# Kernel optimization log

Hardware: AMD Instinct MI355X
Metric: run time of the kernel (lower is better)

Reference implementation:

```python
import jax, jax.numpy as jnp
import numpy as np

D_MODEL = 1024


def setup_inputs() -> dict:
    key = jax.random.key(0)
    ks = jax.random.split(key, 11)
    B, S, D = 4, 2048, D_MODEL
    scale = 1.0 / np.sqrt(D)
    inp = {
        "query": jax.random.normal(ks[0], (B, S, D), dtype=jnp.float32),
        "key": jax.random.normal(ks[1], (B, S, D), dtype=jnp.float32),
        "value": jax.random.normal(ks[2], (B, S, D), dtype=jnp.float32),
        # nn.Linear weights stored torch-style as [out, in]; y = x @ W.T + b
        "Wq": jax.random.normal(ks[3], (D, D), dtype=jnp.float32) * scale,
        "bq": jnp.zeros((D,), dtype=jnp.float32),
        "Wk": jax.random.normal(ks[4], (D, D), dtype=jnp.float32) * scale,
        "bk": jnp.zeros((D,), dtype=jnp.float32),
        "Wv": jax.random.normal(ks[5], (D, D), dtype=jnp.float32) * scale,
        "bv": jnp.zeros((D,), dtype=jnp.float32),
        "Wo": jax.random.normal(ks[6], (D, D), dtype=jnp.float32) * scale,
        "bo": jnp.zeros((D,), dtype=jnp.float32),
    }
    return inp


def reference(query, key, value, Wq, bq, Wk, bk, Wv, bv, Wo, bo):
    d_model = query.shape[-1]
    q = jnp.einsum("bsd,ed->bse", query, Wq) + bq  # q_proj
    k = jnp.einsum("bsd,ed->bse", key, Wk) + bk    # k_proj
    v = jnp.einsum("bsd,ed->bse", value, Wv) + bv  # v_proj
    # scores scaled by sqrt(d_model) (single head: full d_model, per original code)
    scores = jnp.einsum("bqe,bke->bqk", q, k) / jnp.sqrt(jnp.asarray(d_model, q.dtype))
    attn = jax.nn.softmax(scores, axis=-1)
    # dropout is identity in eval mode
    out = jnp.einsum("bqk,bke->bqe", attn, v)
    out = jnp.einsum("bqe,fe->bqf", out, Wo) + bo  # out_proj
    return out
```

## Files before the change

kernel.cpp:

```cpp
#include <hip/hip_runtime.h>
#include <stdint.h>


typedef __bf16  bf16x8 __attribute__((ext_vector_type(8)));
typedef float   f32x4  __attribute__((ext_vector_type(4)));
typedef unsigned int u32x4 __attribute__((ext_vector_type(4)));

__device__ __forceinline__ unsigned short bf16_rne(float f) {
  unsigned int u = __builtin_bit_cast(unsigned int, f);
  u += 0x7FFFu + ((u >> 16) & 1u);
  return (unsigned short)(u >> 16);
}
__device__ __forceinline__ unsigned int pack2(float a, float b) {
  return (unsigned int)bf16_rne(a) | ((unsigned int)bf16_rne(b) << 16);
}
__device__ __forceinline__ void async16(const unsigned short* g, unsigned short* l) {
  __builtin_amdgcn_global_load_lds(
      (const __attribute__((address_space(1))) unsigned int*)g,
      (__attribute__((address_space(3))) unsigned int*)l,
      16, 0, 0);
}

#define FENCE() asm volatile("" ::: "memory")
#define BAR()   __builtin_amdgcn_s_barrier()
#define MFMA_   __builtin_amdgcn_mfma_f32_16x16x32_bf16

#define T1_ARGS() \
  const int xcd = orig & 7, loc = orig >> 3; \
  const int qq  = nwg >> 3, rr = nwg & 7; \
  const int w   = (xcd < rr ? xcd * (qq + 1) : rr * (qq + 1) + (xcd - rr) * qq) + loc; \
  const int bxi = w % nx; \
  const int byi = (w / nx) % ny; \
  const int bzi = w / (nx * ny);

template<int OUT_F32>
__device__ __forceinline__ void gbody256(
    unsigned short* __restrict__ lds,
    const unsigned short* __restrict__ A, const unsigned short* __restrict__ B,
    void* __restrict__ Cp,
    int K, int lda, int ldb, int ldc,
    long sAz, long sBz, long sCz, long sBiasZ,
    float scale, const float* __restrict__ bias, int bias_mode,
    int nx, int ny, int nwg, int orig)
{
  T1_ARGS();

  const int tid  = threadIdx.x;
  const int lane = tid & 63;
  const int wid  = tid >> 6;
  const int bm   = byi * 256;
  const int bn   = bxi * 256;
  const long z   = bzi;

  const unsigned short* Az = A + z * sAz;
  const unsigned short* Bz = B + z * sBz;

  const int wm  = wid >> 2;
  const int wn  = wid & 3;
  const int al  = lane & 15;
  const int ah  = lane >> 4;
  const int al7 = lane & 7;

  const int swz = ((lane & 7) ^ ((lane >> 3) & 7)) << 3;
  const unsigned short* Apt = Az + (long)(bm + wid * 32 + (lane >> 3)) * lda + swz;
  const unsigned short* Bpt = Bz + (long)(bn + wid * 32 + (lane >> 3)) * ldb + swz;
  const long a8 = (long)lda * 8, b8 = (long)ldb * 8;

#define SALL(kt, stg) { \
    const unsigned short* pa_ = Apt + ((long)(kt) << 6); \
    const unsigned short* pb_ = Bpt + ((long)(kt) << 6); \
    async16(pa_,          (stg) + wid * 2048);        \
    async16(pa_ + a8,     (stg) + wid * 2048 + 512);  \
    async16(pa_ + 2 * a8, (stg) + wid * 2048 + 1024); \
    async16(pa_ + 3 * a8, (stg) + wid * 2048 + 1536); \
    async16(pb_,          (stg) + 16384 + wid * 2048);        \
    async16(pb_ + b8,     (stg) + 16384 + wid * 2048 + 512);  \
    async16(pb_ + 2 * b8, (stg) + 16384 + wid * 2048 + 1024); \
    async16(pb_ + 3 * b8, (stg) + 16384 + wid * 2048 + 1536); }

#define LDA2(v0, v1, mm) { const int r_ = (wm * 128 + (mm) * 16 + al) * 64; \
    v0 = *(const bf16x8*)&as[r_ + ((ah ^ al7) << 3)]; \
    v1 = *(const bf16x8*)&as[r_ + (((4 | ah) ^ al7) << 3)]; }
#define LDB2(v0, v1, nn) { const int r_ = (wn * 64 + (nn) * 16 + al) * 64; \
    v0 = *(const bf16x8*)&bs[r_ + ((ah ^ al7) << 3)]; \
    v1 = *(const bf16x8*)&bs[r_ + (((4 | ah) ^ al7) << 3)]; }
#define MM2(mi, ni, av0, av1, bv0, bv1) { \
    acc[mi][ni] = MFMA_(av0, bv0, acc[mi][ni], 0, 0, 0); \
    acc[mi][ni] = MFMA_(av1, bv1, acc[mi][ni], 0, 0, 0); }

  f32x4 acc[8][4] = {};
  const int nkt = K >> 6;

  SALL(0, lds);

  int cur = 0;
  for (int t = 0; t < nkt; ++t) {
    asm volatile("s_waitcnt vmcnt(0)" ::: "memory");
    BAR(); FENCE();

    const unsigned short* as  = lds + cur * 32768;
    const unsigned short* bs  = as + 16384;
    unsigned short*       stg = lds + (cur ^ 1) * 32768;

    bf16x8 a0k0, a0k1, a1k0, a1k1, a2k0, a2k1, a3k0, a3k1;
    bf16x8 a4k0, a4k1, a5k0, a5k1, a6k0, a6k1, a7k0, a7k1;
    bf16x8 b0k0, b0k1, b1k0, b1k1, b2k0, b2k1, b3k0, b3k1;
    LDA2(a0k0, a0k1, 0); LDA2(a1k0, a1k1, 1); LDA2(a2k0, a2k1, 2); LDA2(a3k0, a3k1, 3);
    LDA2(a4k0, a4k1, 4); LDA2(a5k0, a5k1, 5); LDA2(a6k0, a6k1, 6); LDA2(a7k0, a7k1, 7);
    LDB2(b0k0, b0k1, 0); LDB2(b1k0, b1k1, 1); LDB2(b2k0, b2k1, 2); LDB2(b3k0, b3k1, 3);

    if (t + 1 < nkt) SALL(t + 1, stg);

    MM2(0,0, a0k0,a0k1, b0k0,b0k1); MM2(1,0, a1k0,a1k1, b0k0,b0k1);
    MM2(2,0, a2k0,a2k1, b0k0,b0k1); MM2(3,0, a3k0,a3k1, b0k0,b0k1);
    MM2(4,0, a4k0,a4k1, b0k0,b0k1); MM2(5,0, a5k0,a5k1, b0k0,b0k1);
    MM2(6,0, a6k0,a6k1, b0k0,b0k1); MM2(7,0, a7k0,a7k1, b0k0,b0k1);
    MM2(0,1, a0k0,a0k1, b1k0,b1k1); MM2(1,1, a1k0,a1k1, b1k0,b1k1);
    MM2(2,1, a2k0,a2k1, b1k0,b1k1); MM2(3,1, a3k0,a3k1, b1k0,b1k1);
    MM2(4,1, a4k0,a4k1, b1k0,b1k1); MM2(5,1, a5k0,a5k1, b1k0,b1k1);
    MM2(6,1, a6k0,a6k1, b1k0,b1k1); MM2(7,1, a7k0,a7k1, b1k0,b1k1);
    MM2(0,2, a0k0,a0k1, b2k0,b2k1); MM2(1,2, a1k0,a1k1, b2k0,b2k1);
    MM2(2,2, a2k0,a2k1, b2k0,b2k1); MM2(3,2, a3k0,a3k1, b2k0,b2k1);
    MM2(4,2, a4k0,a4k1, b2k0,b2k1); MM2(5,2, a5k0,a5k1, b2k0,b2k1);
    MM2(6,2, a6k0,a6k1, b2k0,b2k1); MM2(7,2, a7k0,a7k1, b2k0,b2k1);
    MM2(0,3, a0k0,a0k1, b3k0,b3k1); MM2(1,3, a1k0,a1k1, b3k0,b3k1);
    MM2(2,3, a2k0,a2k1, b3k0,b3k1); MM2(3,3, a3k0,a3k1, b3k0,b3k1);
    MM2(4,3, a4k0,a4k1, b3k0,b3k1); MM2(5,3, a5k0,a5k1, b3k0,b3k1);
    MM2(6,3, a6k0,a6k1, b3k0,b3k1); MM2(7,3, a7k0,a7k1, b3k0,b3k1);

    cur ^= 1;
  }

  #pragma unroll
  for (int m = 0; m < 8; ++m) {
    #pragma unroll
    for (int n = 0; n < 4; ++n) {
      #pragma unroll
      for (int j = 0; j < 4; ++j) {
        const int grow = bm + wm * 128 + m * 16 + ah * 4 + j;
        const int gcol = bn + wn * 64 + n * 16 + al;
        float v = acc[m][n][j] * scale;
        if (bias_mode == 1)      v += bias[z * sBiasZ + gcol];
        else if (bias_mode == 2) v += bias[z * sBiasZ + grow];
        const long idx = z * sCz + (long)grow * ldc + gcol;
        if (OUT_F32) ((float*)Cp)[idx] = v;
        else         ((unsigned short*)Cp)[idx] = bf16_rne(v);
      }
    }
  }
}

template<int OUT_F32>
__device__ __forceinline__ void gbody8(
    unsigned short* __restrict__ lds,
    const unsigned short* __restrict__ A, const unsigned short* __restrict__ B,
    void* __restrict__ Cp,
    int K, int lda, int ldb, int ldc,
    long sAz, long sBz, long sCz, long sBiasZ,
    float scale, const float* __restrict__ bias, int bias_mode,
    int nx, int ny, int nwg, int orig)
{
  T1_ARGS();

  const int tid  = threadIdx.x;
  const int lane = tid & 63;
  const int wid  = tid >> 6;
  const int bm   = byi * 256;
  const int bn   = bxi * 128;
  const long z   = bzi;

  const unsigned short* Az = A + z * sAz;
  const unsigned short* Bz = B + z * sBz;

  const int wr  = (wid >> 1) * 64;
  const int wc  = (wid & 1)  * 64;
  const int al  = lane & 15;
  const int ah  = lane >> 4;
  const int al7 = lane & 7;

  const int swz = ((lane & 7) ^ ((lane >> 3) & 7)) << 3;
  const unsigned short* Apt = Az + (long)(bm + wid * 32 + (lane >> 3)) * lda + swz;
  const unsigned short* Bpt = Bz + (long)(bn + wid * 16 + (lane >> 3)) * ldb + swz;
  const long a8 = (long)lda * 8, b8 = (long)ldb * 8;

  f32x4 acc[4][4] = {};
  const int nkt = K >> 6;

#define STAGE_AB(kt, stg) { \
    const unsigned short* a_ = Apt + ((long)(kt) << 6); \
    const unsigned short* b_ = Bpt + ((long)(kt) << 6); \
    async16(a_,          (stg) + wid * 2048);        \
    async16(a_ + a8,     (stg) + wid * 2048 + 512);  \
    async16(a_ + 2 * a8, (stg) + wid * 2048 + 1024); \
    async16(a_ + 3 * a8, (stg) + wid * 2048 + 1536); \
    async16(b_,          (stg) + 16384 + wid * 1024); \
    async16(b_ + b8,     (stg) + 16384 + wid * 1024 + 512); }

#define LDA_(m) { const int r_ = (wr + (m) * 16 + al) * 64; \
    af##m##0 = *(const bf16x8*)&as[r_ + ((ah ^ al7) << 3)]; \
    af##m##1 = *(const bf16x8*)&as[r_ + (((4 | ah) ^ al7) << 3)]; }
#define LDB_(n) { const int r_ = (wc + (n) * 16 + al) * 64; \
    bf##n##0 = *(const bf16x8*)&bs[r_ + ((ah ^ al7) << 3)]; \
    bf##n##1 = *(const bf16x8*)&bs[r_ + (((4 | ah) ^ al7) << 3)]; }
#define MM(m, n) { \
    acc[m][n] = MFMA_(af##m##0, bf##n##0, acc[m][n], 0, 0, 0); \
    acc[m][n] = MFMA_(af##m##1, bf##n##1, acc[m][n], 0, 0, 0); }

  STAGE_AB(0, lds);
  STAGE_AB(1, lds + 24576);

  int cur = 0;
  for (int t = 0; t < nkt; ++t) {
    const int stb  = (cur >= 1) ? cur - 1 : cur + 2;

    if (t + 1 < nkt) asm volatile("s_waitcnt vmcnt(6)" ::: "memory");
    else             asm volatile("s_waitcnt vmcnt(0)" ::: "memory");
    BAR(); FENCE();

    const unsigned short* as  = lds + cur * 24576;
    const unsigned short* bs  = as + 16384;
    unsigned short*       stg = lds + stb * 24576;

    bf16x8 af00, af01, af10, af11, af20, af21, af30, af31;
    bf16x8 bf00, bf01, bf10, bf11, bf20, bf21, bf30, bf31;
    LDA_(0); LDA_(1); LDA_(2); LDA_(3);
    LDB_(0); LDB_(1); LDB_(2); LDB_(3);

    if (t + 2 < nkt) STAGE_AB(t + 2, stg);

    MM(0,0); MM(1,0); MM(2,0); MM(3,0);
    MM(0,1); MM(1,1); MM(2,1); MM(3,1);
    MM(0,2); MM(1,2); MM(2,2); MM(3,2);
    MM(0,3); MM(1,3); MM(2,3); MM(3,3);

    cur = (cur == 2) ? 0 : cur + 1;
  }

  #pragma unroll
  for (int m = 0; m < 4; ++m) {
    #pragma unroll
    for (int n = 0; n < 4; ++n) {
      #pragma unroll
      for (int j = 0; j < 4; ++j) {
        const int grow = bm + wr + m * 16 + ah * 4 + j;
        const int gcol = bn + wc + n * 16 + al;
        float v = acc[m][n][j] * scale;
        if (bias_mode == 1)      v += bias[z * sBiasZ + gcol];
        else if (bias_mode == 2) v += bias[z * sBiasZ + grow];
        const long idx = z * sCz + (long)grow * ldc + gcol;
        if (OUT_F32) ((float*)Cp)[idx] = v;
        else         ((unsigned short*)Cp)[idx] = bf16_rne(v);
      }
    }
  }
}

template<int OUT_F32>
__global__ __launch_bounds__(512) void gemm256(
    const unsigned short* __restrict__ A, const unsigned short* __restrict__ B,
    void* __restrict__ Cp, int K, int lda, int ldb, int ldc,
    long sAz, long sBz, long sCz, long sBiasZ,
    float scale, const float* __restrict__ bias, int bias_mode)
{
  __shared__ unsigned short lds[2 * 32768];
  const int nx = gridDim.x, ny = gridDim.y;
  const int nwg = nx * ny * gridDim.z;
  const int orig = ((int)blockIdx.z * ny + blockIdx.y) * nx + blockIdx.x;
  gbody256<OUT_F32>(lds, A, B, Cp, K, lda, ldb, ldc, sAz, sBz, sCz, sBiasZ,
                    scale, bias, bias_mode, nx, ny, nwg, orig);
}

template<int OUT_F32>
__global__ __launch_bounds__(512) void gemm8(
    const unsigned short* __restrict__ A, const unsigned short* __restrict__ B,
    void* __restrict__ Cp, int K, int lda, int ldb, int ldc,
    long sAz, long sBz, long sCz, long sBiasZ,
    float scale, const float* __restrict__ bias, int bias_mode)
{
  __shared__ unsigned short lds[3 * 24576];
  const int nx = gridDim.x, ny = gridDim.y;
  const int nwg = nx * ny * gridDim.z;
  const int orig = ((int)blockIdx.z * ny + blockIdx.y) * nx + blockIdx.x;
  gbody8<OUT_F32>(lds, A, B, Cp, K, lda, ldb, ldc, sAz, sBz, sCz, sBiasZ,
                  scale, bias, bias_mode, nx, ny, nwg, orig);
}

__global__ __launch_bounds__(512) void dual_qk_vt(
    const unsigned short* __restrict__ qf, const unsigned short* __restrict__ Wb,
    unsigned short* __restrict__ q, const float* __restrict__ bqk,
    const unsigned short* __restrict__ Wv, const unsigned short* __restrict__ vf,
    unsigned short* __restrict__ vT, const float* __restrict__ bv)
{
  __shared__ unsigned short lds[3 * 24576];
  const int bid = blockIdx.x;
  if (bid < 256) {
    gbody256<0>(lds, qf, Wb, q, 1024, 1024, 1024, 1024,
                8388608L, 1048576L, 8388608L, 1024L, 1.0f, bqk, 1,
                4, 32, 256, bid);
  } else {
    gbody8<0>(lds, Wv, vf, vT, 1024, 1024, 1024, 8192,
              0L, 0L, 0L, 0L, 1.0f, bv, 2,
              64, 4, 256, bid - 256);
  }
}

__device__ __forceinline__ void cvt8(const float* in, unsigned short* out, long i) {
  f32x4 a = *(const f32x4*)(in + i * 8);
  f32x4 b = *(const f32x4*)(in + i * 8 + 4);
  u32x4 w;
  w[0] = pack2(a[0], a[1]); w[1] = pack2(a[2], a[3]);
  w[2] = pack2(b[0], b[1]); w[3] = pack2(b[2], b[3]);
  *(u32x4*)(out + i * 8) = w;
}

__global__ __launch_bounds__(256) void mega_cvt3(
    const float* __restrict__ wq, const float* __restrict__ wk,
    const float* __restrict__ wv, const float* __restrict__ wo,
    const float* __restrict__ query, const float* __restrict__ key_,
    const float* __restrict__ value,
    const float* __restrict__ bq, const float* __restrict__ bk,
    unsigned short* __restrict__ Wb, unsigned short* __restrict__ qf,
    unsigned short* __restrict__ kf, unsigned short* __restrict__ vf,
    float* __restrict__ bqk)
{
  const int b = blockIdx.x;
  if (b < 2048) {
    const long i = (long)(b & 511) * 256 + threadIdx.x;
    if (b < 512)        cvt8(wq, Wb,            i);
    else if (b < 1024)  cvt8(wk, Wb + 1048576,  i);
    else if (b < 1536)  cvt8(wv, Wb + 2097152,  i);
    else                cvt8(wo, Wb + 3145728,  i);
  } else if (b < 6144) {
    cvt8(query, qf, (long)(b - 2048) * 256 + threadIdx.x);
  } else if (b < 10240) {
    cvt8(key_,  kf, (long)(b - 6144) * 256 + threadIdx.x);
  } else if (b < 10248) {
    const int t = (b - 10240) * 256 + threadIdx.x;
    if (t < 1024) bqk[t] = bq[t];
    else          bqk[t] = bk[t - 1024];
  } else {
    cvt8(value, vf, (long)(b - 10248) * 256 + threadIdx.x);
  }
}

__global__ __launch_bounds__(256) void cvt_f32_bf16(
    const float* __restrict__ in, unsigned short* __restrict__ out, int n8)
{
  const int i = blockIdx.x * 256 + threadIdx.x;
  if (i >= n8) return;
  cvt8(in, out, i);
}

__global__ __launch_bounds__(256) void softmax_inplace(unsigned short* __restrict__ P) {
  const long row = blockIdx.x;
  unsigned short* pr = P + row * 2048;
  const int tid = threadIdx.x;

  u32x4 raw = *(const u32x4*)&pr[tid * 8];
  float s[8];
  #pragma unroll
  for (int i = 0; i < 4; ++i) {
    unsigned int u = raw[i];
    s[2 * i]     = __builtin_bit_cast(float, u << 16);
    s[2 * i + 1] = __builtin_bit_cast(float, u & 0xFFFF0000u);
  }
  float m = s[0];
  #pragma unroll
  for (int i = 1; i < 8; ++i) m = fmaxf(m, s[i]);
  #pragma unroll
  for (int off = 32; off >= 1; off >>= 1) m = fmaxf(m, __shfl_xor(m, off));

  __shared__ float redm[4], reds[4];
  const int wid = tid >> 6, lane = tid & 63;
  if (lane == 0) redm[wid] = m;
  __syncthreads();
  m = fmaxf(fmaxf(redm[0], redm[1]), fmaxf(redm[2], redm[3]));

  float e[8], sum = 0.f;
  #pragma unroll
  for (int i = 0; i < 8; ++i) { e[i] = __expf(s[i] - m); sum += e[i]; }
  #pragma unroll
  for (int off = 32; off >= 1; off >>= 1) sum += __shfl_xor(sum, off);
  if (lane == 0) reds[wid] = sum;
  __syncthreads();
  sum = reds[0] + reds[1] + reds[2] + reds[3];
  const float inv = 1.0f / sum;

  u32x4 outw;
  #pragma unroll
  for (int i = 0; i < 4; ++i) outw[i] = pack2(e[2 * i] * inv, e[2 * i + 1] * inv);
  *(u32x4*)&pr[tid * 8] = outw;
}

extern "C" void kernel_launch(void* const* d_in, const int* in_sizes, int n_in,
                              void* d_out, int out_size, void* d_ws, size_t ws_size,
                              hipStream_t stream) {
  const float* query = (const float*)d_in[0];
  const float* key_  = (const float*)d_in[1];
  const float* value = (const float*)d_in[2];
  const float* Wq    = (const float*)d_in[3];
  const float* bq    = (const float*)d_in[4];
  const float* Wk    = (const float*)d_in[5];
  const float* bk    = (const float*)d_in[6];
  const float* Wv    = (const float*)d_in[7];
  const float* bv    = (const float*)d_in[8];
  const float* Wo    = (const float*)d_in[9];
  const float* bo    = (const float*)d_in[10];

  unsigned short* ws = (unsigned short*)d_ws;
  unsigned short* qf = ws;
  unsigned short* kf = ws + 8388608;
  unsigned short* P  = ws;
  unsigned short* q  = ws + 16777216;
  unsigned short* vT = ws + 33554432;
  unsigned short* Wb = ws + 41943040;
  float*          bqk= (float*)(ws + 46137344);
  unsigned short* o  = q;

  const bool par = ws_size >= (size_t)(46141440 + 8388608) * 2;
  unsigned short* vf = par ? (ws + 46141440) : ws;

  const dim3 blk(256), blk8(512);

  mega_cvt3<<<dim3(par ? 14344 : 10248), blk, 0, stream>>>(
      Wq, Wk, Wv, Wo, query, key_, value, bq, bk, Wb, qf, kf, vf, bqk);

  if (par) {
    dual_qk_vt<<<dim3(512), blk8, 0, stream>>>(qf, Wb, q, bqk,
                                               Wb + 2097152, vf, vT, bv);
  } else {
    gemm256<0><<<dim3(4, 32, 2), blk8, 0, stream>>>(qf, Wb, q,
        1024, 1024, 1024, 1024, 8388608L, 1048576L, 8388608L, 1024L, 1.0f, bqk, 1);
    cvt_f32_bf16<<<dim3(4096), blk, 0, stream>>>(value, vf, 1048576);
    gemm8<0><<<dim3(64, 4, 1), blk8, 0, stream>>>(Wb + 2097152, vf, vT,
        1024, 1024, 1024, 8192, 0L, 0L, 0L, 0L, 1.0f, bv, 2);
  }

  gemm256<0><<<dim3(8, 8, 4), blk8, 0, stream>>>(q, q + 8388608, P,
      1024, 1024, 1024, 2048, 2097152L, 2097152L, 4194304L, 0L, 0.03125f, nullptr, 0);

  softmax_inplace<<<dim3(8192), blk, 0, stream>>>(P);

  gemm8<0><<<dim3(8, 8, 4), blk8, 0, stream>>>(P, vT, o,
      2048, 2048, 8192, 1024, 4194304L, 2048L, 2097152L, 0L, 1.0f, nullptr, 0);

  gemm8<1><<<dim3(8, 32, 1), blk8, 0, stream>>>(o, Wb + 3145728, d_out,
      1024, 1024, 1024, 1024, 0L, 0L, 0L, 0L, 1.0f, bo, 1);
}
```

Measured before the change: 200.9 us.

## Fold output projection into value by precomputing V·Woᵀ before attention

Uses associativity, (P·V)·Woᵀ = P·(V·Woᵀ), to fold the output projection into the value path. The V projection now yields row-major v. A new fused kernel computes the QK scores alongside the transposed product W2T = (V·Woᵀ)ᵀ, so the separate P·V and output-projection GEMMs become one P·W2T GEMM with bias, written in fp32 straight to the output. This removes one full GEMM launch and the round trip of the intermediate o tensor. The cost is an extra 8192x1024x1024 GEMM moved earlier and an added bf16 rounding of V·Woᵀ, which changes numerics slightly.

```diff
diff --git a/kernel.cpp b/kernel.cpp
--- a/kernel.cpp
+++ b/kernel.cpp
@@ -285,11 +285,11 @@
                   scale, bias, bias_mode, nx, ny, nwg, orig);
 }
 
-__global__ __launch_bounds__(512) void dual_qk_vt(
+__global__ __launch_bounds__(512) void dual_qk_v(
     const unsigned short* __restrict__ qf, const unsigned short* __restrict__ Wb,
     unsigned short* __restrict__ q, const float* __restrict__ bqk,
-    const unsigned short* __restrict__ Wv, const unsigned short* __restrict__ vf,
-    unsigned short* __restrict__ vT, const float* __restrict__ bv)
+    const unsigned short* __restrict__ vf, const unsigned short* __restrict__ Wv,
+    unsigned short* __restrict__ v, const float* __restrict__ bv)
 {
   __shared__ unsigned short lds[3 * 24576];
   const int bid = blockIdx.x;
@@ -298,8 +298,27 @@
                 8388608L, 1048576L, 8388608L, 1024L, 1.0f, bqk, 1,
                 4, 32, 256, bid);
   } else {
-    gbody8<0>(lds, Wv, vf, vT, 1024, 1024, 1024, 8192,
-              0L, 0L, 0L, 0L, 1.0f, bv, 2,
+    gbody8<0>(lds, vf, Wv, v, 1024, 1024, 1024, 1024,
+              0L, 0L, 0L, 0L, 1.0f, bv, 1,
+              8, 32, 256, bid - 256);
+  }
+}
+
+__global__ __launch_bounds__(512) void dual_sc_w2(
+    const unsigned short* __restrict__ q, const unsigned short* __restrict__ k,
+    unsigned short* __restrict__ P,
+    const unsigned short* __restrict__ Wo, const unsigned short* __restrict__ v,
+    unsigned short* __restrict__ W2T)
+{
+  __shared__ unsigned short lds[3 * 24576];
+  const int bid = blockIdx.x;
+  if (bid < 256) {
+    gbody256<0>(lds, q, k, P, 1024, 1024, 1024, 2048,
+                2097152L, 2097152L, 4194304L, 0L, 0.03125f, nullptr, 0,
+                8, 8, 256, bid);
+  } else {
+    gbody8<0>(lds, Wo, v, W2T, 1024, 1024, 1024, 8192,
+              0L, 0L, 0L, 0L, 1.0f, nullptr, 0,
               64, 4, 256, bid - 256);
   }
 }
@@ -412,13 +431,14 @@
   unsigned short* kf = ws + 8388608;
   unsigned short* P  = ws;
   unsigned short* q  = ws + 16777216;
-  unsigned short* vT = ws + 33554432;
+  unsigned short* v  = ws + 33554432;
   unsigned short* Wb = ws + 41943040;
   float*          bqk= (float*)(ws + 46137344);
   unsigned short* o  = q;
 
   const bool par = ws_size >= (size_t)(46141440 + 8388608) * 2;
-  unsigned short* vf = par ? (ws + 46141440) : ws;
+  unsigned short* vf  = par ? (ws + 46141440) : ws;
+  unsigned short* W2T = ws + 46141440;
 
   const dim3 blk(256), blk8(512);
 
@@ -426,24 +446,25 @@
       Wq, Wk, Wv, Wo, query, key_, value, bq, bk, Wb, qf, kf, vf, bqk);
 
   if (par) {
-    dual_qk_vt<<<dim3(512), blk8, 0, stream>>>(qf, Wb, q, bqk,
-                                               Wb + 2097152, vf, vT, bv);
+    dual_qk_v<<<dim3(512), blk8, 0, stream>>>(qf, Wb, q, bqk,
+                                              vf, Wb + 2097152, v, bv);
+    dual_sc_w2<<<dim3(512), blk8, 0, stream>>>(q, q + 8388608, P,
+                                               Wb + 3145728, v, W2T);
+    softmax_inplace<<<dim3(8192), blk, 0, stream>>>(P);
+    gemm8<1><<<dim3(8, 8, 4), blk8, 0, stream>>>(P, W2T, d_out,
+        2048, 2048, 8192, 1024, 4194304L, 2048L, 2097152L, 0L, 1.0f, bo, 1);
   } else {
     gemm256<0><<<dim3(4, 32, 2), blk8, 0, stream>>>(qf, Wb, q,
         1024, 1024, 1024, 1024, 8388608L, 1048576L, 8388608L, 1024L, 1.0f, bqk, 1);
     cvt_f32_bf16<<<dim3(4096), blk, 0, stream>>>(value, vf, 1048576);
-    gemm8<0><<<dim3(64, 4, 1), blk8, 0, stream>>>(Wb + 2097152, vf, vT,
+    gemm8<0><<<dim3(64, 4, 1), blk8, 0, stream>>>(Wb + 2097152, vf, v,
         1024, 1024, 1024, 8192, 0L, 0L, 0L, 0L, 1.0f, bv, 2);
-  }
-
-  gemm256<0><<<dim3(8, 8, 4), blk8, 0, stream>>>(q, q + 8388608, P,
-      1024, 1024, 1024, 2048, 2097152L, 2097152L, 4194304L, 0L, 0.03125f, nullptr, 0);
-
-  softmax_inplace<<<dim3(8192), blk, 0, stream>>>(P);
-
-  gemm8<0><<<dim3(8, 8, 4), blk8, 0, stream>>>(P, vT, o,
-      2048, 2048, 8192, 1024, 4194304L, 2048L, 2097152L, 0L, 1.0f, nullptr, 0);
-
-  gemm8<1><<<dim3(8, 32, 1), blk8, 0, stream>>>(o, Wb + 3145728, d_out,
-      1024, 1024, 1024, 1024, 0L, 0L, 0L, 0L, 1.0f, bo, 1);
-}
+    gemm256<0><<<dim3(8, 8, 4), blk8, 0, stream>>>(q, q + 8388608, P,
+        1024, 1024, 1024, 2048, 2097152L, 2097152L, 4194304L, 0L, 0.03125f, nullptr, 0);
+    softmax_inplace<<<dim3(8192), blk, 0, stream>>>(P);
+    gemm8<0><<<dim3(8, 8, 4), blk8, 0, stream>>>(P, v, o,
+        2048, 2048, 8192, 1024, 4194304L, 2048L, 2097152L, 0L, 1.0f, nullptr, 0);
+    gemm8<1><<<dim3(8, 32, 1), blk8, 0, stream>>>(o, Wb + 3145728, d_out,
+        1024, 1024, 1024, 1024, 0L, 0L, 0L, 0L, 1.0f, bo, 1);
+  }
+}
```

Result: faster. 191.0 us (median of 2 runs) (-4.9%).
